# Kernel optimization log

Measured on AMD Instinct MI355X. Metric: run time of the kernel, lower is better.

The kernel has to match this reference:

```python
import jax, jax.numpy as jnp
import numpy as np

N_NODES = 50000
N_EDGES = 800000
D_IN = 128
H = 4
F = 16


def setup_inputs() -> dict:
    key = jax.random.key(0)
    k1, k2, k3, k4 = jax.random.split(key, 4)
    feat = jax.random.normal(k1, (N_NODES, D_IN), dtype=jnp.float32)
    W = jax.random.normal(k2, (D_IN, H * F), dtype=jnp.float32) / np.sqrt(D_IN)
    src = jax.random.randint(k3, (N_EDGES,), 0, N_NODES, dtype=jnp.int32)
    dst = jax.random.randint(k4, (N_EDGES,), 0, N_NODES, dtype=jnp.int32)
    return {"feat": feat, "W": W, "src": src, "dst": dst}


def reference(feat, W, src, dst):
    # Project: [N, D_in] @ [D_in, H*F] -> [N, H, F]
    ft = (feat @ W).reshape(N_NODES, H, F)
    # Per-edge dot-product scores, scaled: [E, H]
    e = jnp.einsum('ehf,ehf->eh', ft[src], ft[dst]) / np.sqrt(F).astype(np.float32)
    # Segment (per-destination) softmax over incoming edges
    seg_max = jax.ops.segment_max(e, dst, num_segments=N_NODES)  # [N, H]
    ex = jnp.exp(e - seg_max[dst])
    denom = jax.ops.segment_sum(ex, dst, num_segments=N_NODES)  # [N, H]
    sa = ex / denom[dst]  # [E, H]
    # Weighted scatter-sum of source features: [N, H, F]
    msgs = ft[src] * sa[:, :, None]
    out = jax.ops.segment_sum(msgs, dst, num_segments=N_NODES)
    return out
```

## Files before the change

### kernel.cpp

```cpp
#include <hip/hip_runtime.h>
#include <hip/hip_fp16.h>

#define N_NODES 50000
#define N_EDGES 800000
#define D_IN 128
#define HH 4
#define FF 16
#define HF 64
#define NBUCKETS 196
#define BCAP 4608
#define CHUNK 2048
#define NBIN_BLOCKS ((N_EDGES + CHUNK - 1) / CHUNK)
#define GEMM_BLOCKS ((N_NODES + 63) / 64)

struct __align__(8) Half4 { __half2 a, b; };

__global__ __launch_bounds__(256, 2) void gemm_kernel(const float* __restrict__ feat,
                                                      const float* __restrict__ W,
                                                      __half* __restrict__ fth) {
    __shared__ float As[64][132];
    __shared__ float Bs[D_IN][HF];

    {
        const float4* W4 = (const float4*)W;
        float4* B4 = (float4*)Bs;
#pragma unroll
        for (int i = 0; i < 8; ++i) {
            int idx = threadIdx.x + 256 * i;
            B4[idx] = W4[idx];
        }
    }
    {
        int row0 = blockIdx.x * 64;
        const float4* F4 = (const float4*)feat;
#pragma unroll
        for (int i = 0; i < 8; ++i) {
            int idx = threadIdx.x + 256 * i;
            int r = idx >> 5;
            int c4 = idx & 31;
            float4 v = make_float4(0.f, 0.f, 0.f, 0.f);
            int row = row0 + r;
            if (row < N_NODES) v = F4[(size_t)row * 32 + c4];
            *(float4*)&As[r][c4 * 4] = v;
        }
    }
    __syncthreads();

    const int tr = threadIdx.x >> 4;
    const int tc = threadIdx.x & 15;

    float acc[4][4] = {};
#pragma unroll 8
    for (int k = 0; k < D_IN; k += 4) {
        float av[4][4], bv[4][4];
#pragma unroll
        for (int i = 0; i < 4; ++i) {
            float4 a = *(const float4*)&As[tr * 4 + i][k];
            av[i][0] = a.x; av[i][1] = a.y; av[i][2] = a.z; av[i][3] = a.w;
        }
#pragma unroll
        for (int j = 0; j < 4; ++j) {
            float4 b = *(const float4*)&Bs[k + j][tc * 4];
            bv[j][0] = b.x; bv[j][1] = b.y; bv[j][2] = b.z; bv[j][3] = b.w;
        }
#pragma unroll
        for (int i = 0; i < 4; ++i)
#pragma unroll
            for (int j = 0; j < 4; ++j)
#pragma unroll
                for (int c = 0; c < 4; ++c)
                    acc[i][c] = fmaf(av[i][j], bv[j][c], acc[i][c]);
    }

    int row0 = blockIdx.x * 64;
#pragma unroll
    for (int i = 0; i < 4; ++i) {
        int row = row0 + tr * 4 + i;
        if (row < N_NODES) {
            Half4 h;
            h.a = __floats2half2_rn(acc[i][0], acc[i][1]);
            h.b = __floats2half2_rn(acc[i][2], acc[i][3]);
            *(Half4*)&fth[(size_t)row * HF + tc * 4] = h;
        }
    }
}

__global__ __launch_bounds__(256) void bin_kernel(const int* __restrict__ src,
                                                  const int* __restrict__ dst,
                                                  int* __restrict__ gcur,
                                                  int* __restrict__ recs) {
    __shared__ int hist[256];
    __shared__ int offs[256];
    __shared__ int cur[256];
    __shared__ int gbase[256];
    __shared__ int lrec[CHUNK];

    int tid = threadIdx.x;
    int e0 = blockIdx.x * CHUNK;
    int n = N_EDGES - e0; if (n > CHUNK) n = CHUNK;

    hist[tid] = 0;
    __syncthreads();

    int myrec[CHUNK / 256];
    int myb[CHUNK / 256];
#pragma unroll
    for (int k = 0; k < CHUNK / 256; ++k) {
        int idx = tid + k * 256;
        myb[k] = -1;
        if (idx < n) {
            int s = src[e0 + idx];
            int d = dst[e0 + idx];
            int b = d >> 8;
            myrec[k] = s | ((d & 255) << 16) | (b << 24);
            myb[k] = b;
            atomicAdd(&hist[b], 1);
        }
    }
    __syncthreads();

    int val = hist[tid];
    offs[tid] = val;
    __syncthreads();
#pragma unroll
    for (int off = 1; off < 256; off <<= 1) {
        int t = (tid >= off) ? offs[tid - off] : 0;
        __syncthreads();
        offs[tid] += t;
        __syncthreads();
    }
    int excl = offs[tid] - val;
    __syncthreads();
    offs[tid] = excl;
    cur[tid] = excl;
    if (tid < NBUCKETS && val > 0) gbase[tid] = atomicAdd(&gcur[tid], val);
    __syncthreads();

#pragma unroll
    for (int k = 0; k < CHUNK / 256; ++k) {
        if (myb[k] >= 0) {
            int p = atomicAdd(&cur[myb[k]], 1);
            lrec[p] = myrec[k];
        }
    }
    __syncthreads();

    for (int i = tid; i < n; i += 256) {
        int r = lrec[i];
        int b = (r >> 24) & 255;
        int pos = gbase[b] + (i - offs[b]);
        if (pos < BCAP) recs[(size_t)b * BCAP + pos] = r;
    }
}

__global__ __launch_bounds__(256) void sort_kernel(const int* __restrict__ gcur,
                                                   const int* __restrict__ recs,
                                                   int* __restrict__ csr,
                                                   int* __restrict__ row_beg,
                                                   int* __restrict__ row_end) {
    __shared__ int lhist[256];
    __shared__ int loffs[256];
    __shared__ int lcur[256];

    int tid = threadIdx.x;
    int b = blockIdx.x;
    int cnt = gcur[b]; if (cnt > BCAP) cnt = BCAP;
    const int* rp = recs + (size_t)b * BCAP;

    lhist[tid] = 0;
    __syncthreads();
    for (int i = tid; i < cnt; i += 256) atomicAdd(&lhist[(rp[i] >> 16) & 255], 1);
    __syncthreads();

    int val = lhist[tid];
    loffs[tid] = val;
    __syncthreads();
#pragma unroll
    for (int off = 1; off < 256; off <<= 1) {
        int t = (tid >= off) ? loffs[tid - off] : 0;
        __syncthreads();
        loffs[tid] += t;
        __syncthreads();
    }
    int excl = loffs[tid] - val;
    __syncthreads();
    lcur[tid] = excl;
    __syncthreads();

    int base = b * BCAP;
    for (int i = tid; i < cnt; i += 256) {
        int rec = rp[i];
        int p = atomicAdd(&lcur[(rec >> 16) & 255], 1);
        csr[base + p] = rec & 0xFFFF;
    }

    int node = b * 256 + tid;
    if (node < N_NODES) {
        row_beg[node] = base + excl;
        row_end[node] = base + excl + val;
    }
}

__global__ __launch_bounds__(256) void gather_kernel(const __half* __restrict__ fth,
                                                     const int* __restrict__ row_beg,
                                                     const int* __restrict__ row_end,
                                                     const int* __restrict__ csr,
                                                     float* __restrict__ out) {
    int node = __builtin_amdgcn_readfirstlane(blockIdx.x * 4 + (threadIdx.x >> 6));
    int lane = threadIdx.x & 63;
    int hl = lane & 31;
    bool hi = lane >= 32;

    int beg = row_beg[node];
    int end = row_end[node];

    __half2 ftd2 = *(const __half2*)&fth[(size_t)node * HF + 2 * hl];

    float acc0 = 0.0f, acc1 = 0.0f, lsum = 0.0f;

    int i = beg;
    for (; i + 4 <= end; i += 4) {
        int sA0 = csr[i + 0], sB0 = csr[i + 1];
        int sA1 = csr[i + 2], sB1 = csr[i + 3];
        int s0 = hi ? sB0 : sA0;
        int s1 = hi ? sB1 : sA1;
        __half2 v20 = *(const __half2*)&fth[(size_t)s0 * HF + 2 * hl];
        __half2 v21 = *(const __half2*)&fth[(size_t)s1 * HF + 2 * hl];

        __half2 pr0 = __hmul2(ftd2, v20);
        __half2 pr1 = __hmul2(ftd2, v21);
        float p0 = __low2float(pr0) + __high2float(pr0);
        float p1 = __low2float(pr1) + __high2float(pr1);
        p0 += __shfl_xor(p0, 1, 64); p1 += __shfl_xor(p1, 1, 64);
        p0 += __shfl_xor(p0, 2, 64); p1 += __shfl_xor(p1, 2, 64);
        p0 += __shfl_xor(p0, 4, 64); p1 += __shfl_xor(p1, 4, 64);
        float w0 = __expf(p0 * 0.25f);
        float w1 = __expf(p1 * 0.25f);
        acc0 = fmaf(w0, __low2float(v20), acc0);
        acc1 = fmaf(w0, __high2float(v20), acc1);
        acc0 = fmaf(w1, __low2float(v21), acc0);
        acc1 = fmaf(w1, __high2float(v21), acc1);
        lsum += w0 + w1;
    }
    for (; i < end; i += 2) {
        bool hasB = (i + 1 < end);
        int sA = csr[i];
        int sB = hasB ? csr[i + 1] : sA;
        int s = hi ? sB : sA;
        __half2 v2 = *(const __half2*)&fth[(size_t)s * HF + 2 * hl];
        __half2 pr = __hmul2(ftd2, v2);
        float p = __low2float(pr) + __high2float(pr);
        p += __shfl_xor(p, 1, 64);
        p += __shfl_xor(p, 2, 64);
        p += __shfl_xor(p, 4, 64);
        float w = __expf(p * 0.25f);
        if (hi && !hasB) w = 0.0f;
        acc0 = fmaf(w, __low2float(v2), acc0);
        acc1 = fmaf(w, __high2float(v2), acc1);
        lsum += w;
    }

    acc0 += __shfl_xor(acc0, 32, 64);
    acc1 += __shfl_xor(acc1, 32, 64);
    lsum += __shfl_xor(lsum, 32, 64);

    if (!hi) {
        float inv = (lsum > 0.0f) ? 1.0f / lsum : 0.0f;
        *(float2*)&out[(size_t)node * HF + 2 * hl] = make_float2(acc0 * inv, acc1 * inv);
    }
}

extern "C" void kernel_launch(void* const* d_in, const int* in_sizes, int n_in,
                              void* d_out, int out_size, void* d_ws, size_t ws_size,
                              hipStream_t stream) {
    const float* feat = (const float*)d_in[0];
    const float* W = (const float*)d_in[1];
    const int* src = (const int*)d_in[2];
    const int* dst = (const int*)d_in[3];
    float* out = (float*)d_out;

    __half* fth = (__half*)d_ws;
    int* recs = (int*)(fth + (size_t)N_NODES * HF);
    int* csr = recs + (size_t)NBUCKETS * BCAP;
    int* row_beg = csr + (size_t)NBUCKETS * BCAP;
    int* row_end = row_beg + N_NODES;
    int* gcur = row_end + N_NODES;

    hipMemsetAsync(gcur, 0, NBUCKETS * sizeof(int), stream);
    gemm_kernel<<<GEMM_BLOCKS, 256, 0, stream>>>(feat, W, fth);
    bin_kernel<<<NBIN_BLOCKS, 256, 0, stream>>>(src, dst, gcur, recs);
    sort_kernel<<<NBUCKETS, 256, 0, stream>>>(gcur, recs, csr, row_beg, row_end);
    gather_kernel<<<N_NODES * 64 / 256, 256, 0, stream>>>(fth, row_beg, row_end, csr, out);
}
```

Baseline: 149.1 us.

## Build compact CSR via degree count and global scan; widen gather to 8 edges per step

The per-bucket local sort is replaced with a global degree histogram (atomics in bin_kernel), a three-kernel prefix scan, and an atomic-cursor scatter into a compact CSR with a single row_ptr array. The gather kernel now gives each lane 4 halves and processes 8 edges per iteration using packed fp16 dot instructions, with masking instead of a separate tail loop. The bin chunk size is also halved to launch more blocks. This adds three small kernel launches and many global atomics on the degree and cursor arrays, in exchange for more edge-level parallelism in the gather and a cheaper sort stage.

New measurement: 197.2 us. 1.32x slower.

```diff
diff --git a/kernel.cpp b/kernel.cpp
--- a/kernel.cpp
+++ b/kernel.cpp
@@ -9,11 +9,25 @@
 #define HF 64
 #define NBUCKETS 196
 #define BCAP 4608
-#define CHUNK 2048
+#define CHUNK 1024
 #define NBIN_BLOCKS ((N_EDGES + CHUNK - 1) / CHUNK)
+#define NBLK_SCAN ((N_NODES + 255) / 256)
 #define GEMM_BLOCKS ((N_NODES + 63) / 64)
 
 struct __align__(8) Half4 { __half2 a, b; };
+
+typedef _Float16 half2_v __attribute__((ext_vector_type(2)));
+struct __align__(8) H4 { half2_v a, b; };
+
+__device__ __forceinline__ float dot4h(H4 a, H4 v) {
+#if __has_builtin(__builtin_amdgcn_fdot2)
+    return __builtin_amdgcn_fdot2(a.a, v.a,
+           __builtin_amdgcn_fdot2(a.b, v.b, 0.0f, false), false);
+#else
+    return (float)a.a[0] * (float)v.a[0] + (float)a.a[1] * (float)v.a[1]
+         + (float)a.b[0] * (float)v.b[0] + (float)a.b[1] * (float)v.b[1];
+#endif
+}
 
 __global__ __launch_bounds__(256, 2) void gemm_kernel(const float* __restrict__ feat,
                                                       const float* __restrict__ W,
@@ -88,7 +102,8 @@
 __global__ __launch_bounds__(256) void bin_kernel(const int* __restrict__ src,
                                                   const int* __restrict__ dst,
                                                   int* __restrict__ gcur,
-                                                  int* __restrict__ recs) {
+                                                  int* __restrict__ recs,
+                                                  int* __restrict__ deg) {
     __shared__ int hist[256];
     __shared__ int offs[256];
     __shared__ int cur[256];
@@ -115,6 +130,7 @@
             myrec[k] = s | ((d & 255) << 16) | (b << 24);
             myb[k] = b;
             atomicAdd(&hist[b], 1);
+            atomicAdd(&deg[d], 1);
         }
     }
     __syncthreads();
@@ -153,120 +169,129 @@
     }
 }
 
-__global__ __launch_bounds__(256) void sort_kernel(const int* __restrict__ gcur,
-                                                   const int* __restrict__ recs,
-                                                   int* __restrict__ csr,
-                                                   int* __restrict__ row_beg,
-                                                   int* __restrict__ row_end) {
-    __shared__ int lhist[256];
-    __shared__ int loffs[256];
-    __shared__ int lcur[256];
-
+__global__ __launch_bounds__(256) void scan1_kernel(const int* __restrict__ deg,
+                                                    int* __restrict__ row_ptr,
+                                                    int* __restrict__ block_sums) {
+    __shared__ int s[256];
     int tid = threadIdx.x;
-    int b = blockIdx.x;
+    int i = blockIdx.x * 256 + tid;
+    int val = (i < N_NODES) ? deg[i] : 0;
+    s[tid] = val;
+    __syncthreads();
+#pragma unroll
+    for (int off = 1; off < 256; off <<= 1) {
+        int t = (tid >= off) ? s[tid - off] : 0;
+        __syncthreads();
+        s[tid] += t;
+        __syncthreads();
+    }
+    if (i < N_NODES) row_ptr[i] = s[tid] - val;
+    if (tid == 255) block_sums[blockIdx.x] = s[255];
+}
+
+__global__ __launch_bounds__(256) void scan2_kernel(int* __restrict__ block_sums) {
+    __shared__ int s[256];
+    int tid = threadIdx.x;
+    int val = (tid < NBLK_SCAN) ? block_sums[tid] : 0;
+    s[tid] = val;
+    __syncthreads();
+#pragma unroll
+    for (int off = 1; off < 256; off <<= 1) {
+        int t = (tid >= off) ? s[tid - off] : 0;
+        __syncthreads();
+        s[tid] += t;
+        __syncthreads();
+    }
+    if (tid < NBLK_SCAN) block_sums[tid] = s[tid] - val;
+}
+
+__global__ __launch_bounds__(256) void scan3_kernel(int* __restrict__ row_ptr,
+                                                    const int* __restrict__ block_sums,
+                                                    int* __restrict__ cursor) {
+    int tid = threadIdx.x;
+    int i = blockIdx.x * 256 + tid;
+    if (i < N_NODES) {
+        int v = row_ptr[i] + block_sums[blockIdx.x];
+        row_ptr[i] = v;
+        cursor[i] = v;
+    }
+    if (blockIdx.x == 0 && tid == 0) row_ptr[N_NODES] = N_EDGES;
+}
+
+__global__ __launch_bounds__(256) void scatter_kernel(const int* __restrict__ gcur,
+                                                      const int* __restrict__ recs,
+                                                      int* __restrict__ cursor,
+                                                      int* __restrict__ csr) {
+    int j = blockIdx.x;
+    int b = j >> 2;
+    int q = j & 3;
     int cnt = gcur[b]; if (cnt > BCAP) cnt = BCAP;
+    int lo = q * (BCAP / 4);
+    int hi = lo + (BCAP / 4); if (hi > cnt) hi = cnt;
     const int* rp = recs + (size_t)b * BCAP;
-
-    lhist[tid] = 0;
-    __syncthreads();
-    for (int i = tid; i < cnt; i += 256) atomicAdd(&lhist[(rp[i] >> 16) & 255], 1);
-    __syncthreads();
-
-    int val = lhist[tid];
-    loffs[tid] = val;
-    __syncthreads();
-#pragma unroll
-    for (int off = 1; off < 256; off <<= 1) {
-        int t = (tid >= off) ? loffs[tid - off] : 0;
-        __syncthreads();
-        loffs[tid] += t;
-        __syncthreads();
-    }
-    int excl = loffs[tid] - val;
-    __syncthreads();
-    lcur[tid] = excl;
-    __syncthreads();
-
-    int base = b * BCAP;
-    for (int i = tid; i < cnt; i += 256) {
+    for (int i = lo + threadIdx.x; i < hi; i += 256) {
         int rec = rp[i];
-        int p = atomicAdd(&lcur[(rec >> 16) & 255], 1);
-        csr[base + p] = rec & 0xFFFF;
-    }
-
-    int node = b * 256 + tid;
-    if (node < N_NODES) {
-        row_beg[node] = base + excl;
-        row_end[node] = base + excl + val;
+        int node = (b << 8) + ((rec >> 16) & 255);
+        int p = atomicAdd(&cursor[node], 1);
+        csr[p] = rec & 0xFFFF;
     }
 }
 
 __global__ __launch_bounds__(256) void gather_kernel(const __half* __restrict__ fth,
-                                                     const int* __restrict__ row_beg,
-                                                     const int* __restrict__ row_end,
+                                                     const int* __restrict__ row_ptr,
                                                      const int* __restrict__ csr,
                                                      float* __restrict__ out) {
     int node = __builtin_amdgcn_readfirstlane(blockIdx.x * 4 + (threadIdx.x >> 6));
     int lane = threadIdx.x & 63;
-    int hl = lane & 31;
-    bool hi = lane >= 32;
-
-    int beg = row_beg[node];
-    int end = row_end[node];
-
-    __half2 ftd2 = *(const __half2*)&fth[(size_t)node * HF + 2 * hl];
-
-    float acc0 = 0.0f, acc1 = 0.0f, lsum = 0.0f;
-
-    int i = beg;
-    for (; i + 4 <= end; i += 4) {
-        int sA0 = csr[i + 0], sB0 = csr[i + 1];
-        int sA1 = csr[i + 2], sB1 = csr[i + 3];
-        int s0 = hi ? sB0 : sA0;
-        int s1 = hi ? sB1 : sA1;
-        __half2 v20 = *(const __half2*)&fth[(size_t)s0 * HF + 2 * hl];
-        __half2 v21 = *(const __half2*)&fth[(size_t)s1 * HF + 2 * hl];
-
-        __half2 pr0 = __hmul2(ftd2, v20);
-        __half2 pr1 = __hmul2(ftd2, v21);
-        float p0 = __low2float(pr0) + __high2float(pr0);
-        float p1 = __low2float(pr1) + __high2float(pr1);
-        p0 += __shfl_xor(p0, 1, 64); p1 += __shfl_xor(p1, 1, 64);
-        p0 += __shfl_xor(p0, 2, 64); p1 += __shfl_xor(p1, 2, 64);
-        p0 += __shfl_xor(p0, 4, 64); p1 += __shfl_xor(p1, 4, 64);
-        float w0 = __expf(p0 * 0.25f);
-        float w1 = __expf(p1 * 0.25f);
-        acc0 = fmaf(w0, __low2float(v20), acc0);
-        acc1 = fmaf(w0, __high2float(v20), acc1);
-        acc0 = fmaf(w1, __low2float(v21), acc0);
-        acc1 = fmaf(w1, __high2float(v21), acc1);
+    int g = lane >> 4;
+    int hl = lane & 15;
+
+    int beg = row_ptr[node];
+    int end = row_ptr[node + 1];
+
+    H4 a = *(const H4*)&fth[(size_t)node * HF + 4 * hl];
+
+    float acc0 = 0.f, acc1 = 0.f, acc2 = 0.f, acc3 = 0.f, lsum = 0.f;
+
+    for (int i = beg; i < end; i += 8) {
+        int idx0 = i + g;
+        int idx1 = i + 4 + g;
+        bool act0 = idx0 < end;
+        bool act1 = idx1 < end;
+        int s0 = csr[act0 ? idx0 : beg];
+        int s1 = csr[act1 ? idx1 : beg];
+        H4 v0 = *(const H4*)&fth[(size_t)s0 * HF + 4 * hl];
+        H4 v1 = *(const H4*)&fth[(size_t)s1 * HF + 4 * hl];
+
+        float p0 = dot4h(a, v0);
+        float p1 = dot4h(a, v1);
+        p0 += __shfl_xor(p0, 1, 64);  p1 += __shfl_xor(p1, 1, 64);
+        p0 += __shfl_xor(p0, 2, 64);  p1 += __shfl_xor(p1, 2, 64);
+
+        float w0 = act0 ? __expf(p0 * 0.25f) : 0.0f;
+        float w1 = act1 ? __expf(p1 * 0.25f) : 0.0f;
+
+        acc0 = fmaf(w0, (float)v0.a[0], acc0);
+        acc1 = fmaf(w0, (float)v0.a[1], acc1);
+        acc2 = fmaf(w0, (float)v0.b[0], acc2);
+        acc3 = fmaf(w0, (float)v0.b[1], acc3);
+        acc0 = fmaf(w1, (float)v1.a[0], acc0);
+        acc1 = fmaf(w1, (float)v1.a[1], acc1);
+        acc2 = fmaf(w1, (float)v1.b[0], acc2);
+        acc3 = fmaf(w1, (float)v1.b[1], acc3);
         lsum += w0 + w1;
     }
-    for (; i < end; i += 2) {
-        bool hasB = (i + 1 < end);
-        int sA = csr[i];
-        int sB = hasB ? csr[i + 1] : sA;
-        int s = hi ? sB : sA;
-        __half2 v2 = *(const __half2*)&fth[(size_t)s * HF + 2 * hl];
-        __half2 pr = __hmul2(ftd2, v2);
-        float p = __low2float(pr) + __high2float(pr);
-        p += __shfl_xor(p, 1, 64);
-        p += __shfl_xor(p, 2, 64);
-        p += __shfl_xor(p, 4, 64);
-        float w = __expf(p * 0.25f);
-        if (hi && !hasB) w = 0.0f;
-        acc0 = fmaf(w, __low2float(v2), acc0);
-        acc1 = fmaf(w, __high2float(v2), acc1);
-        lsum += w;
-    }
-
-    acc0 += __shfl_xor(acc0, 32, 64);
-    acc1 += __shfl_xor(acc1, 32, 64);
-    lsum += __shfl_xor(lsum, 32, 64);
-
-    if (!hi) {
+
+    acc0 += __shfl_xor(acc0, 16, 64);  acc0 += __shfl_xor(acc0, 32, 64);
+    acc1 += __shfl_xor(acc1, 16, 64);  acc1 += __shfl_xor(acc1, 32, 64);
+    acc2 += __shfl_xor(acc2, 16, 64);  acc2 += __shfl_xor(acc2, 32, 64);
+    acc3 += __shfl_xor(acc3, 16, 64);  acc3 += __shfl_xor(acc3, 32, 64);
+    lsum += __shfl_xor(lsum, 16, 64);  lsum += __shfl_xor(lsum, 32, 64);
+
+    if (lane < 16) {
         float inv = (lsum > 0.0f) ? 1.0f / lsum : 0.0f;
-        *(float2*)&out[(size_t)node * HF + 2 * hl] = make_float2(acc0 * inv, acc1 * inv);
+        *(float4*)&out[(size_t)node * HF + 4 * hl] =
+            make_float4(acc0 * inv, acc1 * inv, acc2 * inv, acc3 * inv);
     }
 }
 
@@ -282,13 +307,18 @@
     __half* fth = (__half*)d_ws;
     int* recs = (int*)(fth + (size_t)N_NODES * HF);
     int* csr = recs + (size_t)NBUCKETS * BCAP;
-    int* row_beg = csr + (size_t)NBUCKETS * BCAP;
-    int* row_end = row_beg + N_NODES;
-    int* gcur = row_end + N_NODES;
-
-    hipMemsetAsync(gcur, 0, NBUCKETS * sizeof(int), stream);
+    int* deg = csr + N_EDGES;
+    int* gcur = deg + N_NODES;
+    int* row_ptr = gcur + NBUCKETS;
+    int* cursor = row_ptr + N_NODES + 1;
+    int* block_sums = cursor + N_NODES;
+
+    hipMemsetAsync(deg, 0, (N_NODES + NBUCKETS) * sizeof(int), stream);
     gemm_kernel<<<GEMM_BLOCKS, 256, 0, stream>>>(feat, W, fth);
-    bin_kernel<<<NBIN_BLOCKS, 256, 0, stream>>>(src, dst, gcur, recs);
-    sort_kernel<<<NBUCKETS, 256, 0, stream>>>(gcur, recs, csr, row_beg, row_end);
-    gather_kernel<<<N_NODES * 64 / 256, 256, 0, stream>>>(fth, row_beg, row_end, csr, out);
-}
+    bin_kernel<<<NBIN_BLOCKS, 256, 0, stream>>>(src, dst, gcur, recs, deg);
+    scan1_kernel<<<NBLK_SCAN, 256, 0, stream>>>(deg, row_ptr, block_sums);
+    scan2_kernel<<<1, 256, 0, stream>>>(block_sums);
+    scan3_kernel<<<NBLK_SCAN, 256, 0, stream>>>(row_ptr, block_sums, cursor);
+    scatter_kernel<<<NBUCKETS * 4, 256, 0, stream>>>(gcur, recs, cursor, csr);
+    gather_kernel<<<N_NODES * 64 / 256, 256, 0, stream>>>(fth, row_ptr, csr, out);
+}
```
